# Kernel optimization log

Measured on AMD Instinct MI355X. Metric: run time of the kernel, lower is better.

The kernel has to match this reference:

```python
import jax, jax.numpy as jnp
import numpy as np

HEADS = 16
DIM_HEAD = 64
LN_EPS = 1e-5


def _layernorm(x, gamma, beta):
    mu = jnp.mean(x, axis=-1, keepdims=True)
    var = jnp.mean(jnp.square(x - mu), axis=-1, keepdims=True)
    return (x - mu) * jax.lax.rsqrt(var + LN_EPS) * gamma + beta


def setup_inputs() -> dict:
    key = jax.random.key(0)
    k1, k2, k3 = jax.random.split(key, 3)
    B, N, D = 4, 2048, 1024
    inner = HEADS * DIM_HEAD  # 1024
    x = jax.random.normal(k1, (B, N, D), dtype=jnp.float32)
    ln_gamma = jnp.ones((D,), dtype=jnp.float32)
    ln_beta = jnp.zeros((D,), dtype=jnp.float32)
    w_qkv = jax.random.normal(k2, (3 * inner, D), dtype=jnp.float32) * (1.0 / np.sqrt(D))
    w_out = jax.random.normal(k3, (D, inner), dtype=jnp.float32) * (1.0 / np.sqrt(inner))
    b_out = jnp.zeros((D,), dtype=jnp.float32)
    return {"x": x, "ln_gamma": ln_gamma, "ln_beta": ln_beta,
            "w_qkv": w_qkv, "w_out": w_out, "b_out": b_out}


def reference(x, ln_gamma, ln_beta, w_qkv, w_out, b_out):
    B, N, D = x.shape
    h, d = HEADS, DIM_HEAD
    xn = _layernorm(x, ln_gamma, ln_beta)
    qkv = xn @ w_qkv.T  # [B, N, 3*inner]
    q, k, v = jnp.split(qkv, 3, axis=-1)
    q = q.reshape(B, N, h, d)
    k = k.reshape(B, N, h, d)
    v = v.reshape(B, N, h, d)
    scale = 1.0 / np.sqrt(d)  # TET uses 1/sqrt(E); tau=1, delta=0, no mask
    scores = jnp.einsum('blhe,bshe->bhls', q, k)
    A = jax.nn.softmax(scale * scores, axis=-1)  # [B, H, N, N]
    out = jnp.einsum('bhls,bshd->blhd', A, v).reshape(B, N, h * d)
    return out @ w_out.T + b_out
```

## Files before the change

### kernel.cpp

```cpp
#include <hip/hip_runtime.h>

typedef unsigned short ushortT;
typedef __attribute__((ext_vector_type(8))) short short8;
typedef __attribute__((ext_vector_type(4))) float f32x4;

#define QSCALE 0.18033688011112042f

__device__ __forceinline__ ushortT f2bf(float f) {
  union { float f; unsigned int u; } v; v.f = f;
  unsigned int r = v.u + 0x7FFFu + ((v.u >> 16) & 1u);
  return (ushortT)(r >> 16);
}

__device__ __forceinline__ unsigned int pk2bf(float a, float b) {
  union { float f; unsigned int u; } ua, ub; ua.f = a; ub.f = b;
  return __builtin_amdgcn_perm(ub.u + 0x8000u, ua.u + 0x8000u, 0x07060302u);
}

__device__ __forceinline__ void pl_swap(unsigned int& a, unsigned int& b) {
  asm("v_permlane32_swap_b32 %0, %1" : "+v"(a), "+v"(b));
  asm("v_permlane16_swap_b32 %0, %1" : "+v"(a), "+v"(b));
}

__device__ __forceinline__ void gld_lds16(const void* g, void* l) {
  __builtin_amdgcn_global_load_lds(
      (const __attribute__((address_space(1))) unsigned int*)g,
      (__attribute__((address_space(3))) unsigned int*)l, 16, 0, 0);
}

__global__ __launch_bounds__(256) void cvt_kernel(const float* __restrict__ src,
                                                  ushortT* __restrict__ dst, int n4) {
  int i = blockIdx.x * 256 + threadIdx.x;
  if (i < n4) {
    float4 v = ((const float4*)src)[i];
    ushort4 o;
    o.x = f2bf(v.x); o.y = f2bf(v.y); o.z = f2bf(v.z); o.w = f2bf(v.w);
    ((ushort4*)dst)[i] = o;
  }
}

__global__ __launch_bounds__(256) void ln_kernel(const float* __restrict__ x,
                                                 const float* __restrict__ g,
                                                 const float* __restrict__ be,
                                                 ushortT* __restrict__ xn) {
  const int row = blockIdx.x, tid = threadIdx.x;
  const float4 v = ((const float4*)(x + (size_t)row * 1024))[tid];
  float s1 = v.x + v.y + v.z + v.w;
  float s2 = v.x * v.x + v.y * v.y + v.z * v.z + v.w * v.w;
#pragma unroll
  for (int off = 32; off >= 1; off >>= 1) {
    s1 += __shfl_xor(s1, off, 64);
    s2 += __shfl_xor(s2, off, 64);
  }
  __shared__ float red[8];
  const int wave = tid >> 6, lane = tid & 63;
  if (lane == 0) { red[wave] = s1; red[4 + wave] = s2; }
  __syncthreads();
  s1 = red[0] + red[1] + red[2] + red[3];
  s2 = red[4] + red[5] + red[6] + red[7];
  const float mean = s1 * (1.0f / 1024.0f);
  const float var  = s2 * (1.0f / 1024.0f) - mean * mean;
  const float rs = rsqrtf(var + 1e-5f);
  const float4 gv = ((const float4*)g)[tid];
  const float4 bv = ((const float4*)be)[tid];
  ushort4 o;
  o.x = f2bf((v.x - mean) * rs * gv.x + bv.x);
  o.y = f2bf((v.y - mean) * rs * gv.y + bv.y);
  o.z = f2bf((v.z - mean) * rs * gv.z + bv.z);
  o.w = f2bf((v.w - mean) * rs * gv.w + bv.w);
  ((ushort4*)xn)[(size_t)row * 256 + tid] = o;
}

template <int MODE>
__global__ __launch_bounds__(256, 2) void gemm_bt(
    const ushortT* __restrict__ A, const ushortT* __restrict__ Bm,
    int M, int N, int K,
    ushortT* __restrict__ qbuf, ushortT* __restrict__ kbuf, ushortT* __restrict__ vbuf,
    float* __restrict__ outf, const float* __restrict__ bias) {
  __shared__ ushortT lds_a[128 * 64];
  __shared__ ushortT lds_b[128 * 64];
  const int tid = threadIdx.x;
  const int wave = tid >> 6, lane = tid & 63;
  const int q4 = lane >> 4, l16 = lane & 15;
  const int m0 = blockIdx.y * 128, n0 = blockIdx.x * 128;
  const int wm = (wave >> 1) * 64, wn = (wave & 1) * 64;
  const int srow = lane >> 3;
  const int scol = ((lane & 7) ^ srow) * 8;
  const int sw = l16 & 7;

  f32x4 acc[4][4];
#pragma unroll
  for (int i = 0; i < 4; i++)
#pragma unroll
    for (int j = 0; j < 4; j++) acc[i][j] = (f32x4){0.f, 0.f, 0.f, 0.f};

  for (int k0 = 0; k0 < K; k0 += 64) {
#pragma unroll
    for (int j = 0; j < 4; j++) {
      const int q = wave * 4 + j;
      gld_lds16(&A[(size_t)(m0 + q * 8 + srow) * K + (k0 + scol)], &lds_a[q * 512]);
      gld_lds16(&Bm[(size_t)(n0 + q * 8 + srow) * K + (k0 + scol)], &lds_b[q * 512]);
    }
    __syncthreads();
#pragma unroll
    for (int kk = 0; kk < 2; kk++) {
      short8 af[4], bf[4];
#pragma unroll
      for (int i = 0; i < 4; i++)
        af[i] = *(const short8*)&lds_a[(wm + i * 16 + l16) * 64 + ((kk * 4 + q4) ^ sw) * 8];
#pragma unroll
      for (int i = 0; i < 4; i++)
        bf[i] = *(const short8*)&lds_b[(wn + i * 16 + l16) * 64 + ((kk * 4 + q4) ^ sw) * 8];
#pragma unroll
      for (int im = 0; im < 4; im++)
#pragma unroll
        for (int in = 0; in < 4; in++)
          acc[im][in] = __builtin_amdgcn_mfma_f32_16x16x32_bf16(af[im], bf[in], acc[im][in], 0, 0, 0);
    }
    __syncthreads();
  }

#pragma unroll
  for (int im = 0; im < 4; im++) {
    const int grow_base = m0 + wm + im * 16 + q4 * 4;
#pragma unroll
    for (int in = 0; in < 4; in++) {
      const int c = n0 + wn + in * 16 + l16;
#pragma unroll
      for (int r = 0; r < 4; r++) {
        const float v = acc[im][in][r];
        const int grow = grow_base + r;
        if (MODE == 0) {
          outf[(size_t)grow * N + c] = v + bias[c];
        } else {
          const int which = c >> 10;
          const int h = (c >> 6) & 15;
          const int d = c & 63;
          const int b = grow >> 11, n = grow & 2047;
          if (which == 0) {
            qbuf[((size_t)(b * 16 + h) * 2048 + n) * 64 + d] = f2bf(v * QSCALE);
          } else if (which == 1) {
            kbuf[((size_t)(b * 16 + h) * 2048 + n) * 64 + d] = f2bf(v);
          } else {
            vbuf[((size_t)(b * 16 + h) * 64 + d) * 2048 + n] = f2bf(v);
          }
        }
      }
    }
  }
}

__global__ __launch_bounds__(256, 2) void attn_kernel(
    const ushortT* __restrict__ Qb, const ushortT* __restrict__ Kb,
    const ushortT* __restrict__ Vt, ushortT* __restrict__ Ob) {
  __shared__ ushortT kb[2][4096];
  __shared__ ushortT vb[2][4096];
  const int tid = threadIdx.x;
  const int wave = tid >> 6, lane = tid & 63;
  const int q4 = lane >> 4, l16 = lane & 15;
  const int sw = l16 & 7;
  const int blk = blockIdx.x;
  const int bh = blk & 63, qt = blk >> 6;
  const ushortT* Qp = Qb + (size_t)bh * (2048 * 64);
  const ushortT* Kp = Kb + (size_t)bh * (2048 * 64);
  const ushortT* Vp = Vt + (size_t)bh * (64 * 2048);
  const int qrow0 = qt * 256 + wave * 64;

  short8 qf[4][2];
#pragma unroll
  for (int qn = 0; qn < 4; qn++)
#pragma unroll
    for (int kk = 0; kk < 2; kk++)
      qf[qn][kk] = *(const short8*)&Qp[(size_t)(qrow0 + qn * 16 + l16) * 64 + kk * 32 + q4 * 8];

  f32x4 acc[4][4];
#pragma unroll
  for (int dn = 0; dn < 4; dn++)
#pragma unroll
    for (int qn = 0; qn < 4; qn++) acc[dn][qn] = (f32x4){0.f, 0.f, 0.f, 0.f};
  float lsum[4] = {0.f, 0.f, 0.f, 0.f};

  const int krow = lane >> 3, kchk = ((lane & 7) ^ (lane >> 3)) * 8;
  const int vrow = tid >> 3, vchk = ((tid & 7) ^ ((tid >> 3) & 7)) * 8;
  auto stage = [&](int buf, int s0) {
    gld_lds16(&Kp[(size_t)(s0 + wave * 8 + krow) * 64 + kchk], &kb[buf][wave * 512]);
    gld_lds16(&Kp[(size_t)(s0 + 32 + wave * 8 + krow) * 64 + kchk], &kb[buf][2048 + wave * 512]);
    gld_lds16(&Vp[(size_t)vrow * 2048 + s0 + vchk], &vb[buf][wave * 512]);
    gld_lds16(&Vp[(size_t)(vrow + 32) * 2048 + s0 + vchk], &vb[buf][2048 + wave * 512]);
  };

  stage(0, 0);

  for (int t = 0; t < 32; t++) {
    const int cur = t & 1;
    __syncthreads();
    if (t < 31) stage(cur ^ 1, (t + 1) * 64);

    f32x4 sa[4][4];
#pragma unroll
    for (int qn = 0; qn < 4; qn++)
#pragma unroll
      for (int cn = 0; cn < 4; cn++) sa[qn][cn] = (f32x4){0.f, 0.f, 0.f, 0.f};
#pragma unroll
    for (int cn = 0; cn < 4; cn++) {
      const short8 kf0 = *(const short8*)&kb[cur][(cn * 16 + l16) * 64 + (q4 ^ sw) * 8];
      const short8 kf1 = *(const short8*)&kb[cur][(cn * 16 + l16) * 64 + ((q4 + 4) ^ sw) * 8];
#pragma unroll
      for (int qn = 0; qn < 4; qn++) {
        sa[qn][cn] = __builtin_amdgcn_mfma_f32_16x16x32_bf16(kf0, qf[qn][0], sa[qn][cn], 0, 0, 0);
        sa[qn][cn] = __builtin_amdgcn_mfma_f32_16x16x32_bf16(kf1, qf[qn][1], sa[qn][cn], 0, 0, 0);
      }
    }

    short8 pf[4][2];
#pragma unroll
    for (int qn = 0; qn < 4; qn++) {
      unsigned int w[4][2];
#pragma unroll
      for (int cn = 0; cn < 4; cn++) {
        float p0 = __builtin_amdgcn_exp2f(sa[qn][cn][0]);
        float p1 = __builtin_amdgcn_exp2f(sa[qn][cn][1]);
        float p2 = __builtin_amdgcn_exp2f(sa[qn][cn][2]);
        float p3 = __builtin_amdgcn_exp2f(sa[qn][cn][3]);
        lsum[qn] += (p0 + p1) + (p2 + p3);
        w[cn][0] = pk2bf(p0, p1);
        w[cn][1] = pk2bf(p2, p3);
      }
#pragma unroll
      for (int ks = 0; ks < 2; ks++) {
        unsigned int a0 = w[2 * ks][0], b0 = w[2 * ks + 1][0];
        unsigned int a1 = w[2 * ks][1], b1 = w[2 * ks + 1][1];
        pl_swap(a0, b0);
        pl_swap(a1, b1);
        union { unsigned int u[4]; short8 s; } tr;
        tr.u[0] = a0; tr.u[1] = a1; tr.u[2] = b0; tr.u[3] = b1;
        pf[qn][ks] = tr.s;
      }
    }

#pragma unroll
    for (int dn = 0; dn < 4; dn++) {
      const short8 vf0 = *(const short8*)&vb[cur][(dn * 16 + l16) * 64 + (q4 ^ sw) * 8];
      const short8 vf1 = *(const short8*)&vb[cur][(dn * 16 + l16) * 64 + ((q4 + 4) ^ sw) * 8];
#pragma unroll
      for (int qn = 0; qn < 4; qn++) {
        acc[dn][qn] = __builtin_amdgcn_mfma_f32_16x16x32_bf16(vf0, pf[qn][0], acc[dn][qn], 0, 0, 0);
        acc[dn][qn] = __builtin_amdgcn_mfma_f32_16x16x32_bf16(vf1, pf[qn][1], acc[dn][qn], 0, 0, 0);
      }
    }
  }

  const int b = bh >> 4, h = bh & 15;
#pragma unroll
  for (int qn = 0; qn < 4; qn++) {
    float l = lsum[qn];
    l += __shfl_xor(l, 16, 64);
    l += __shfl_xor(l, 32, 64);
    const float inv = 1.0f / l;
    const size_t row = (size_t)(b * 2048 + qrow0 + qn * 16 + l16) * 1024 + h * 64;
#pragma unroll
    for (int dn = 0; dn < 4; dn++) {
      ushort4 o;
      o.x = f2bf(acc[dn][qn][0] * inv);
      o.y = f2bf(acc[dn][qn][1] * inv);
      o.z = f2bf(acc[dn][qn][2] * inv);
      o.w = f2bf(acc[dn][qn][3] * inv);
      *(ushort4*)&Ob[row + dn * 16 + q4 * 4] = o;
    }
  }
}

extern "C" void kernel_launch(void* const* d_in, const int* in_sizes, int n_in,
                              void* d_out, int out_size, void* d_ws, size_t ws_size,
                              hipStream_t stream) {
  const float* x    = (const float*)d_in[0];
  const float* g    = (const float*)d_in[1];
  const float* be   = (const float*)d_in[2];
  const float* wqkv = (const float*)d_in[3];
  const float* wout = (const float*)d_in[4];
  const float* bout = (const float*)d_in[5];
  float* out = (float*)d_out;

  char* ws = (char*)d_ws;
  ushortT* xn = (ushortT*)(ws + 0);
  ushortT* wq = (ushortT*)(ws + 16777216);
  ushortT* wo = (ushortT*)(ws + 23068672);
  ushortT* Qb = (ushortT*)(ws + 25165824);
  ushortT* Kb = (ushortT*)(ws + 41943040);
  ushortT* Vt = (ushortT*)(ws + 58720256);
  ushortT* Ob = (ushortT*)(ws + 75497472);

  cvt_kernel<<<3072, 256, 0, stream>>>(wqkv, wq, 786432);
  cvt_kernel<<<1024, 256, 0, stream>>>(wout, wo, 262144);
  ln_kernel<<<8192, 256, 0, stream>>>(x, g, be, xn);
  gemm_bt<1><<<dim3(24, 64), 256, 0, stream>>>(xn, wq, 8192, 3072, 1024,
                                               Qb, Kb, Vt, nullptr, nullptr);
  attn_kernel<<<512, 256, 0, stream>>>(Qb, Kb, Vt, Ob);
  gemm_bt<0><<<dim3(8, 64), 256, 0, stream>>>(Ob, wo, 8192, 1024, 1024,
                                              nullptr, nullptr, nullptr, out, bout);
}
```

Before: 300.3 us.

## Store Q/K row-major interleaved, fold Q scale into weights, vectorize V transpose stores

The QKV GEMM epilogue now writes Q and K directly as a row-major [token, 2048] buffer instead of scattering them into per-head layouts. The attention kernel reads that buffer with a 2048-element stride. The Q scale is folded into the bf16 weight conversion, so the epilogue no longer multiplies Q. V's transposed store now packs bf16 pairs and uses permlane swaps to write 16-byte vectors instead of scalar 2-byte scattered stores. This is meant to cut the cost of the uncoalesced epilogue writes, at the price of strided K/Q loads in attention and a small change in rounding from scaling the weights before bf16 conversion.

```diff
diff --git a/kernel.cpp b/kernel.cpp
--- a/kernel.cpp
+++ b/kernel.cpp
@@ -29,12 +29,14 @@
 }
 
 __global__ __launch_bounds__(256) void cvt_kernel(const float* __restrict__ src,
-                                                  ushortT* __restrict__ dst, int n4) {
+                                                  ushortT* __restrict__ dst, int n4,
+                                                  int qlimit4, float scale) {
   int i = blockIdx.x * 256 + threadIdx.x;
   if (i < n4) {
     float4 v = ((const float4*)src)[i];
+    const float s = (i < qlimit4) ? scale : 1.0f;
     ushort4 o;
-    o.x = f2bf(v.x); o.y = f2bf(v.y); o.z = f2bf(v.z); o.w = f2bf(v.w);
+    o.x = f2bf(v.x * s); o.y = f2bf(v.y * s); o.z = f2bf(v.z * s); o.w = f2bf(v.w * s);
     ((ushort4*)dst)[i] = o;
   }
 }
@@ -75,7 +77,7 @@
 __global__ __launch_bounds__(256, 2) void gemm_bt(
     const ushortT* __restrict__ A, const ushortT* __restrict__ Bm,
     int M, int N, int K,
-    ushortT* __restrict__ qbuf, ushortT* __restrict__ kbuf, ushortT* __restrict__ vbuf,
+    ushortT* __restrict__ qkbuf, ushortT* __restrict__ vbuf,
     float* __restrict__ outf, const float* __restrict__ bias) {
   __shared__ ushortT lds_a[128 * 64];
   __shared__ ushortT lds_b[128 * 64];
@@ -120,39 +122,52 @@
     __syncthreads();
   }
 
-#pragma unroll
-  for (int im = 0; im < 4; im++) {
-    const int grow_base = m0 + wm + im * 16 + q4 * 4;
-#pragma unroll
-    for (int in = 0; in < 4; in++) {
-      const int c = n0 + wn + in * 16 + l16;
-#pragma unroll
-      for (int r = 0; r < 4; r++) {
-        const float v = acc[im][in][r];
-        const int grow = grow_base + r;
-        if (MODE == 0) {
-          outf[(size_t)grow * N + c] = v + bias[c];
-        } else {
-          const int which = c >> 10;
-          const int h = (c >> 6) & 15;
-          const int d = c & 63;
-          const int b = grow >> 11, n = grow & 2047;
-          if (which == 0) {
-            qbuf[((size_t)(b * 16 + h) * 2048 + n) * 64 + d] = f2bf(v * QSCALE);
-          } else if (which == 1) {
-            kbuf[((size_t)(b * 16 + h) * 2048 + n) * 64 + d] = f2bf(v);
-          } else {
-            vbuf[((size_t)(b * 16 + h) * 64 + d) * 2048 + n] = f2bf(v);
-          }
-        }
+  if (MODE == 0) {
+#pragma unroll
+    for (int im = 0; im < 4; im++)
+#pragma unroll
+      for (int in = 0; in < 4; in++) {
+        const int c = n0 + wn + in * 16 + l16;
+#pragma unroll
+        for (int r = 0; r < 4; r++)
+          outf[(size_t)(m0 + wm + im * 16 + q4 * 4 + r) * N + c] = acc[im][in][r] + bias[c];
+      }
+  } else if (n0 < 2048) {
+#pragma unroll
+    for (int im = 0; im < 4; im++)
+#pragma unroll
+      for (int in = 0; in < 4; in++) {
+        const int c = n0 + wn + in * 16 + l16;
+#pragma unroll
+        for (int r = 0; r < 4; r++)
+          qkbuf[(size_t)(m0 + wm + im * 16 + q4 * 4 + r) * 2048 + c] = f2bf(acc[im][in][r]);
+      }
+  } else {
+#pragma unroll
+    for (int j = 0; j < 2; j++) {
+      const int t0 = m0 + wm + j * 32 + q4 * 8;
+      const int b = t0 >> 11, n = t0 & 2047;
+#pragma unroll
+      for (int in = 0; in < 4; in++) {
+        const int cg = n0 - 2048 + wn + in * 16 + l16;
+        const int h = cg >> 6, d = cg & 63;
+        unsigned int a0 = pk2bf(acc[2 * j][in][0], acc[2 * j][in][1]);
+        unsigned int a1 = pk2bf(acc[2 * j][in][2], acc[2 * j][in][3]);
+        unsigned int b0 = pk2bf(acc[2 * j + 1][in][0], acc[2 * j + 1][in][1]);
+        unsigned int b1 = pk2bf(acc[2 * j + 1][in][2], acc[2 * j + 1][in][3]);
+        pl_swap(a0, b0);
+        pl_swap(a1, b1);
+        union { unsigned int u[4]; short8 s; } tr;
+        tr.u[0] = a0; tr.u[1] = a1; tr.u[2] = b0; tr.u[3] = b1;
+        *(short8*)&vbuf[((size_t)((b * 16 + h) * 64 + d)) * 2048 + n] = tr.s;
       }
     }
   }
 }
 
 __global__ __launch_bounds__(256, 2) void attn_kernel(
-    const ushortT* __restrict__ Qb, const ushortT* __restrict__ Kb,
-    const ushortT* __restrict__ Vt, ushortT* __restrict__ Ob) {
+    const ushortT* __restrict__ QK, const ushortT* __restrict__ Vt,
+    ushortT* __restrict__ Ob) {
   __shared__ ushortT kb[2][4096];
   __shared__ ushortT vb[2][4096];
   const int tid = threadIdx.x;
@@ -161,8 +176,9 @@
   const int sw = l16 & 7;
   const int blk = blockIdx.x;
   const int bh = blk & 63, qt = blk >> 6;
-  const ushortT* Qp = Qb + (size_t)bh * (2048 * 64);
-  const ushortT* Kp = Kb + (size_t)bh * (2048 * 64);
+  const int b = bh >> 4, h = bh & 15;
+  const ushortT* Qp = QK + (size_t)b * 2048 * 2048 + h * 64;
+  const ushortT* Kp = Qp + 1024;
   const ushortT* Vp = Vt + (size_t)bh * (64 * 2048);
   const int qrow0 = qt * 256 + wave * 64;
 
@@ -171,7 +187,7 @@
   for (int qn = 0; qn < 4; qn++)
 #pragma unroll
     for (int kk = 0; kk < 2; kk++)
-      qf[qn][kk] = *(const short8*)&Qp[(size_t)(qrow0 + qn * 16 + l16) * 64 + kk * 32 + q4 * 8];
+      qf[qn][kk] = *(const short8*)&Qp[(size_t)(qrow0 + qn * 16 + l16) * 2048 + kk * 32 + q4 * 8];
 
   f32x4 acc[4][4];
 #pragma unroll
@@ -183,8 +199,8 @@
   const int krow = lane >> 3, kchk = ((lane & 7) ^ (lane >> 3)) * 8;
   const int vrow = tid >> 3, vchk = ((tid & 7) ^ ((tid >> 3) & 7)) * 8;
   auto stage = [&](int buf, int s0) {
-    gld_lds16(&Kp[(size_t)(s0 + wave * 8 + krow) * 64 + kchk], &kb[buf][wave * 512]);
-    gld_lds16(&Kp[(size_t)(s0 + 32 + wave * 8 + krow) * 64 + kchk], &kb[buf][2048 + wave * 512]);
+    gld_lds16(&Kp[(size_t)(s0 + wave * 8 + krow) * 2048 + kchk], &kb[buf][wave * 512]);
+    gld_lds16(&Kp[(size_t)(s0 + 32 + wave * 8 + krow) * 2048 + kchk], &kb[buf][2048 + wave * 512]);
     gld_lds16(&Vp[(size_t)vrow * 2048 + s0 + vchk], &vb[buf][wave * 512]);
     gld_lds16(&Vp[(size_t)(vrow + 32) * 2048 + s0 + vchk], &vb[buf][2048 + wave * 512]);
   };
@@ -250,7 +266,6 @@
     }
   }
 
-  const int b = bh >> 4, h = bh & 15;
 #pragma unroll
   for (int qn = 0; qn < 4; qn++) {
     float l = lsum[qn];
@@ -285,17 +300,16 @@
   ushortT* xn = (ushortT*)(ws + 0);
   ushortT* wq = (ushortT*)(ws + 16777216);
   ushortT* wo = (ushortT*)(ws + 23068672);
-  ushortT* Qb = (ushortT*)(ws + 25165824);
-  ushortT* Kb = (ushortT*)(ws + 41943040);
+  ushortT* QK = (ushortT*)(ws + 25165824);
   ushortT* Vt = (ushortT*)(ws + 58720256);
   ushortT* Ob = (ushortT*)(ws + 75497472);
 
-  cvt_kernel<<<3072, 256, 0, stream>>>(wqkv, wq, 786432);
-  cvt_kernel<<<1024, 256, 0, stream>>>(wout, wo, 262144);
+  cvt_kernel<<<3072, 256, 0, stream>>>(wqkv, wq, 786432, 262144, QSCALE);
+  cvt_kernel<<<1024, 256, 0, stream>>>(wout, wo, 262144, 0, 1.0f);
   ln_kernel<<<8192, 256, 0, stream>>>(x, g, be, xn);
   gemm_bt<1><<<dim3(24, 64), 256, 0, stream>>>(xn, wq, 8192, 3072, 1024,
-                                               Qb, Kb, Vt, nullptr, nullptr);
-  attn_kernel<<<512, 256, 0, stream>>>(Qb, Kb, Vt, Ob);
+                                               QK, Vt, nullptr, nullptr);
+  attn_kernel<<<512, 256, 0, stream>>>(QK, Vt, Ob);
   gemm_bt<0><<<dim3(8, 64), 256, 0, stream>>>(Ob, wo, 8192, 1024, 1024,
-                                              nullptr, nullptr, nullptr, out, bout);
-}
+                                              nullptr, nullptr, out, bout);
+}
```

New measurement: 265.7 us. -11.5%, faster.
